# Kernel optimization log

Hardware: AMD Instinct MI355X
Metric: run time of the kernel (lower is better)

The kernel has to match this reference:

```python
import jax, jax.numpy as jnp
import numpy as np

B, T, D = 4, 4096, 1024
H, HD, K = 16, 64, 32
TAU, THRESHOLD, PULSE_BASE, N_STEPS = 0.1, 0.5, 4.0, 5


def setup_inputs() -> dict:
    key = jax.random.key(0)
    ks = jax.random.split(key, 8)
    s = 0.02
    return {
        "x": jax.random.normal(ks[0], (B, T, D), jnp.float32),
        "spectral_basis": jax.random.normal(ks[1], (B, T, K), jnp.float32) / np.sqrt(T),
        "W_qkv": jax.random.normal(ks[2], (3 * D, D), jnp.float32) * s,
        "W_out": jax.random.normal(ks[3], (D, D), jnp.float32) * s,
        "a": jnp.float32(0.7),
        "b": jnp.float32(0.8),
        "W1": jax.random.normal(ks[4], (HD // 2, HD), jnp.float32) * s,
        "b1": jnp.zeros((HD // 2,), jnp.float32),
        "W2": jax.random.normal(ks[5], (1, HD // 2), jnp.float32) * s,
        "b2": jnp.zeros((1,), jnp.float32),
        "spectral_filter": jnp.full((H, 32), 0.5, jnp.float32),
    }


def soliton_dynamics(stimulus, a, b):
    # stimulus: (B, H, K, HD); FitzHugh-Nagumo style 5-step Euler integration
    dt = 1.0 / N_STEPS
    v = jnp.zeros_like(stimulus)
    w = jnp.zeros_like(stimulus)
    stim_scale = jnp.clip(jnp.max(jnp.abs(stimulus), axis=-1, keepdims=True), 1e-06, None)
    stim_n = stimulus / stim_scale
    I = jnp.where(jnp.abs(stimulus) > THRESHOLD, stim_n, stim_n * 0.1)
    for _ in range(N_STEPS):
        dv = v - v ** 3 / 3 - w + I
        dw = (v + a - b * w) / TAU
        v = jnp.clip(v + dt * dv, -3.0, 3.0)
        w = jnp.clip(w + dt * dw, -3.0, 3.0)
    return v * stim_scale, v


def reference(x, spectral_basis, W_qkv, W_out, a, b, W1, b1, W2, b2, spectral_filter):
    Bx, Tx, Dx = x.shape
    k = spectral_basis.shape[-1]
    qkv = x @ W_qkv.T                                   # (B,T,3D)
    qkv = qkv.reshape(Bx, Tx, 3, H, HD).transpose(2, 0, 3, 1, 4)
    q, kk, v = qkv[0], qkv[1], qkv[2]                   # (B,H,T,HD)

    qm = q.mean(axis=2)                                 # (B,H,HD)
    h1 = jax.nn.silu(qm @ W1.T + b1)
    pulse_widths = PULSE_BASE + jax.nn.softplus(h1 @ W2.T + b2)[..., 0]  # (B,H)

    q_spec = jnp.einsum('bhtd,btk->bhkd', q, spectral_basis)
    k_spec = jnp.einsum('bhtd,btk->bhkd', kk, spectral_basis)
    attn_spec = jnp.einsum('bhkd,bhkd->bhk', q_spec, k_spec) / np.sqrt(HD)
    filt = jax.nn.sigmoid(spectral_filter[:, :k])       # (H,k)
    attn_spec = attn_spec * filt[None]

    stim = jnp.broadcast_to(attn_spec[..., None], (Bx, H, k, HD))
    response, state = soliton_dynamics(stim, a, b)
    response = response.mean(axis=-1)                   # (B,H,k)

    v_spec = jnp.einsum('bhtd,btk->bhkd', v, spectral_basis)
    out_spec = response[..., None] * v_spec             # (B,H,k,HD)
    out = jnp.einsum('bhkd,btk->bhtd', out_spec, spectral_basis)
    out = out.transpose(0, 2, 1, 3).reshape(Bx, Tx, Dx)
    out = out @ W_out.T
    return out, pulse_widths, response
```

## Files before the change

### kernel.cpp

```cpp
#include <hip/hip_runtime.h>

#define B_ 4
#define T_ 4096
#define D_ 1024
#define H_ 16
#define K_ 32


__device__ __forceinline__ void fma4(float4& a, float s, const float4& v){
  a.x = fmaf(s, v.x, a.x); a.y = fmaf(s, v.y, a.y);
  a.z = fmaf(s, v.z, a.z); a.w = fmaf(s, v.w, a.w);
}

__global__ __launch_bounds__(256) void reduce_g(
    const float4* __restrict__ src, float4* __restrict__ dst,
    const int n4, const int zper, const int stride4)
{
  const int g = blockIdx.y;
  int i = blockIdx.x * 256 + threadIdx.x;
  if (i >= n4) return;
  float s0 = 0.f, s1 = 0.f, s2 = 0.f, s3 = 0.f;
  const float4* p = src + (size_t)g * zper * stride4 + i;
  #pragma unroll 8
  for (int zz = 0; zz < zper; ++zz){
    float4 v = p[(size_t)zz * stride4];
    s0 += v.x; s1 += v.y; s2 += v.z; s3 += v.w;
  }
  float4 o; o.x = s0; o.y = s1; o.z = s2; o.w = s3;
  dst[(size_t)g * stride4 + i] = o;
}

__global__ __launch_bounds__(256) void reduce_zp(
    const float4* __restrict__ src, float4* __restrict__ dst,
    const int n4, const int z, const int stride4, const int total4)
{
  int i = blockIdx.x * 256 + threadIdx.x;
  if (i >= total4) return;
  if (i >= n4){
    float4 zv; zv.x = 0.f; zv.y = 0.f; zv.z = 0.f; zv.w = 0.f;
    dst[i] = zv; return;
  }
  float s0 = 0.f, s1 = 0.f, s2 = 0.f, s3 = 0.f;
  const float4* p = src + i;
  #pragma unroll 8
  for (int zz = 0; zz < z; ++zz){
    float4 v = p[(size_t)zz * stride4];
    s0 += v.x; s1 += v.y; s2 += v.z; s3 += v.w;
  }
  float4 o; o.x = s0; o.y = s1; o.z = s2; o.w = s3;
  dst[i] = o;
}

__global__ __launch_bounds__(256) void reduce_z(
    const float4* __restrict__ src, float4* __restrict__ dst,
    const int n4, const int z, const int stride4)
{
  int i = blockIdx.x * 256 + threadIdx.x;
  if (i >= n4) return;
  float s0 = 0.f, s1 = 0.f, s2 = 0.f, s3 = 0.f;
  const float4* p = src + i;
  #pragma unroll 8
  for (int zz = 0; zz < z; ++zz){
    float4 v = p[(size_t)zz * stride4];
    s0 += v.x; s1 += v.y; s2 += v.z; s3 += v.w;
  }
  float4 o; o.x = s0; o.y = s1; o.z = s2; o.w = s3;
  dst[i] = o;
}

__global__ __launch_bounds__(256) void k1_spectral_p(
    const float* __restrict__ x, const float* __restrict__ sb,
    float* __restrict__ XP)
{
  const int ct = blockIdx.x;
  const int b  = blockIdx.y;
  const int zz = blockIdx.z;
  const int t0 = zz * 64;
  const int cs = threadIdx.x & 63;
  const int kg = threadIdx.x >> 6;
  __shared__ __align__(16) float4 xt[4096];
  __shared__ __align__(16) float sbs[64][36];
  #pragma unroll
  for (int i = 0; i < 8; i++){
    int idx = threadIdx.x + i * 256;
    int t = idx >> 5, kk = idx & 31;
    sbs[t][kk] = sb[(size_t)(b * T_ + t0 + t) * K_ + kk];
  }
  const float4* xg = (const float4*)(x + (size_t)(b * T_ + t0) * D_ + ct * 256);
  float4 rv[16];
  #pragma unroll
  for (int j = 0; j < 16; j++){
    int idx = threadIdx.x + j * 256;
    int t = idx >> 6, cq = idx & 63;
    rv[j] = xg[(size_t)t * 256 + cq];
  }
  #pragma unroll
  for (int j = 0; j < 16; j++) xt[threadIdx.x + j * 256] = rv[j];
  __syncthreads();

  float4 acc[8];
  #pragma unroll
  for (int k = 0; k < 8; k++){ acc[k].x = 0.f; acc[k].y = 0.f;
                               acc[k].z = 0.f; acc[k].w = 0.f; }
  float4 am; am.x = 0.f; am.y = 0.f; am.z = 0.f; am.w = 0.f;
  #pragma unroll 4
  for (int t = 0; t < 64; ++t){
    float4 xv = xt[t * 64 + cs];
    if (kg == 0){ am.x += xv.x; am.y += xv.y; am.z += xv.z; am.w += xv.w; }
    const float4* srow = (const float4*)&sbs[t][kg * 8];
    float4 s0 = srow[0], s1 = srow[1];
    fma4(acc[0], s0.x, xv); fma4(acc[1], s0.y, xv);
    fma4(acc[2], s0.z, xv); fma4(acc[3], s0.w, xv);
    fma4(acc[4], s1.x, xv); fma4(acc[5], s1.y, xv);
    fma4(acc[6], s1.z, xv); fma4(acc[7], s1.w, xv);
  }
  const int c = ct * 256 + cs * 4;
  float* o = XP + (size_t)zz * 135168 + (size_t)(b * K_ + kg * 8) * D_ + c;
  #pragma unroll
  for (int k = 0; k < 8; k++) *(float4*)(o + (size_t)k * D_) = acc[k];
  if (kg == 0)
    *(float4*)(XP + (size_t)zz * 135168 + 131072 + b * D_ + c) = am;
}

__global__ __launch_bounds__(256) void gemm_qkv(
    const float* __restrict__ A, const float* __restrict__ W,
    float* __restrict__ Cp)
{
  __shared__ __align__(16) float As[64][68];
  __shared__ __align__(16) float Ws[64][132];
  const int nt = blockIdx.x, mt = blockIdx.y;
  const int cb = blockIdx.z * 64;
  const int sc = threadIdx.x & 63, sr = threadIdx.x >> 6;
  {
    const float* Ap = A + (size_t)(mt * 64 + sr) * 1024 + cb + sc;
    float r[16];
    #pragma unroll
    for (int i = 0; i < 16; i++) r[i] = Ap[(size_t)(i * 4) * 1024];
    #pragma unroll
    for (int i = 0; i < 16; i++) As[sc][sr + i * 4] = r[i];
  }
  {
    const float* Wp = W + (size_t)(nt * 128 + sr) * 1024 + cb + sc;
    float r[32];
    #pragma unroll
    for (int i = 0; i < 32; i++) r[i] = Wp[(size_t)(i * 4) * 1024];
    #pragma unroll
    for (int i = 0; i < 32; i++) Ws[sc][sr + i * 4] = r[i];
  }
  __syncthreads();
  const int tx = threadIdx.x & 15, ty = threadIdx.x >> 4;
  float4 acc[4][2];
  #pragma unroll
  for (int i = 0; i < 4; i++)
    #pragma unroll
    for (int j = 0; j < 2; j++){ acc[i][j].x = 0.f; acc[i][j].y = 0.f;
                                 acc[i][j].z = 0.f; acc[i][j].w = 0.f; }
  #pragma unroll 8
  for (int c = 0; c < 64; ++c){
    const float4 a4 = *(const float4*)&As[c][ty * 4];
    const float4 w0 = *(const float4*)&Ws[c][tx * 4];
    const float4 w1 = *(const float4*)&Ws[c][64 + tx * 4];
    fma4(acc[0][0], a4.x, w0); fma4(acc[0][1], a4.x, w1);
    fma4(acc[1][0], a4.y, w0); fma4(acc[1][1], a4.y, w1);
    fma4(acc[2][0], a4.z, w0); fma4(acc[2][1], a4.z, w1);
    fma4(acc[3][0], a4.w, w0); fma4(acc[3][1], a4.w, w1);
  }
  float* cp = Cp + (size_t)blockIdx.z * 589824;
  #pragma unroll
  for (int i = 0; i < 4; i++){
    float* row = cp + (size_t)(mt * 64 + ty * 4 + i) * 3072 + nt * 128;
    *(float4*)(row + tx * 4)      = acc[i][0];
    *(float4*)(row + 64 + tx * 4) = acc[i][1];
  }
}

__global__ __launch_bounds__(256) void gemm_aw_p(
    const float* __restrict__ A, const float* __restrict__ W,
    float* __restrict__ Cp, const int N, const int cPerSplit, const int MN)
{
  __shared__ __align__(16) float As[32][68];
  __shared__ __align__(16) float Ws[32][68];
  const int nt = blockIdx.x, mt = blockIdx.y;
  const int cbase = blockIdx.z * cPerSplit;
  const int tx = threadIdx.x & 15, ty = threadIdx.x >> 4;
  const int sc = threadIdx.x & 31, sr = threadIdx.x >> 5;
  float acc[4][4];
  #pragma unroll
  for (int i = 0; i < 4; i++)
    #pragma unroll
    for (int j = 0; j < 4; j++) acc[i][j] = 0.f;

  float ra[8], rw[8];
  const float* Ap = A + (size_t)(mt * 64 + sr) * 1024 + cbase + sc;
  const float* Wp = W + (size_t)(nt * 64 + sr) * 1024 + cbase + sc;
  #pragma unroll
  for (int i = 0; i < 8; i++){ ra[i] = Ap[(size_t)(i * 8) * 1024];
                               rw[i] = Wp[(size_t)(i * 8) * 1024]; }
  #pragma unroll
  for (int i = 0; i < 8; i++){ As[sc][sr + i * 8] = ra[i];
                               Ws[sc][sr + i * 8] = rw[i]; }
  __syncthreads();

  for (int cc = 32; cc < cPerSplit; cc += 32){
    #pragma unroll
    for (int i = 0; i < 8; i++){ ra[i] = Ap[(size_t)(i * 8) * 1024 + cc];
                                 rw[i] = Wp[(size_t)(i * 8) * 1024 + cc]; }
    #pragma unroll 4
    for (int c = 0; c < 32; ++c){
      const float4 a4 = *(const float4*)&As[c][ty * 4];
      const float4 w4 = *(const float4*)&Ws[c][tx * 4];
      acc[0][0] = fmaf(a4.x, w4.x, acc[0][0]);
      acc[0][1] = fmaf(a4.x, w4.y, acc[0][1]);
      acc[0][2] = fmaf(a4.x, w4.z, acc[0][2]);
      acc[0][3] = fmaf(a4.x, w4.w, acc[0][3]);
      acc[1][0] = fmaf(a4.y, w4.x, acc[1][0]);
      acc[1][1] = fmaf(a4.y, w4.y, acc[1][1]);
      acc[1][2] = fmaf(a4.y, w4.z, acc[1][2]);
      acc[1][3] = fmaf(a4.y, w4.w, acc[1][3]);
      acc[2][0] = fmaf(a4.z, w4.x, acc[2][0]);
      acc[2][1] = fmaf(a4.z, w4.y, acc[2][1]);
      acc[2][2] = fmaf(a4.z, w4.z, acc[2][2]);
      acc[2][3] = fmaf(a4.z, w4.w, acc[2][3]);
      acc[3][0] = fmaf(a4.w, w4.x, acc[3][0]);
      acc[3][1] = fmaf(a4.w, w4.y, acc[3][1]);
      acc[3][2] = fmaf(a4.w, w4.z, acc[3][2]);
      acc[3][3] = fmaf(a4.w, w4.w, acc[3][3]);
    }
    __syncthreads();
    #pragma unroll
    for (int i = 0; i < 8; i++){ As[sc][sr + i * 8] = ra[i];
                                 Ws[sc][sr + i * 8] = rw[i]; }
    __syncthreads();
  }
  #pragma unroll 4
  for (int c = 0; c < 32; ++c){
    const float4 a4 = *(const float4*)&As[c][ty * 4];
    const float4 w4 = *(const float4*)&Ws[c][tx * 4];
    acc[0][0] = fmaf(a4.x, w4.x, acc[0][0]);
    acc[0][1] = fmaf(a4.x, w4.y, acc[0][1]);
    acc[0][2] = fmaf(a4.x, w4.z, acc[0][2]);
    acc[0][3] = fmaf(a4.x, w4.w, acc[0][3]);
    acc[1][0] = fmaf(a4.y, w4.x, acc[1][0]);
    acc[1][1] = fmaf(a4.y, w4.y, acc[1][1]);
    acc[1][2] = fmaf(a4.y, w4.z, acc[1][2]);
    acc[1][3] = fmaf(a4.y, w4.w, acc[1][3]);
    acc[2][0] = fmaf(a4.z, w4.x, acc[2][0]);
    acc[2][1] = fmaf(a4.z, w4.y, acc[2][1]);
    acc[2][2] = fmaf(a4.z, w4.z, acc[2][2]);
    acc[2][3] = fmaf(a4.z, w4.w, acc[2][3]);
    acc[3][0] = fmaf(a4.w, w4.x, acc[3][0]);
    acc[3][1] = fmaf(a4.w, w4.y, acc[3][1]);
    acc[3][2] = fmaf(a4.w, w4.z, acc[3][2]);
    acc[3][3] = fmaf(a4.w, w4.w, acc[3][3]);
  }
  float* cp = Cp + (size_t)blockIdx.z * MN;
  #pragma unroll
  for (int i = 0; i < 4; i++){
    float4 o; o.x = acc[i][0]; o.y = acc[i][1]; o.z = acc[i][2]; o.w = acc[i][3];
    *(float4*)(cp + (size_t)(mt * 64 + ty * 4 + i) * N + nt * 64 + tx * 4) = o;
  }
}

__global__ __launch_bounds__(64) void k3_small(
    const float* __restrict__ qkvC,
    const float* __restrict__ W1, const float* __restrict__ b1,
    const float* __restrict__ W2, const float* __restrict__ b2,
    const float* __restrict__ filt,
    const float* __restrict__ a_in, const float* __restrict__ b_in,
    float* __restrict__ u, float* __restrict__ out_pulse,
    float* __restrict__ out_resp)
{
  const int b = blockIdx.x >> 4, h = blockIdx.x & 15;
  const int d = threadIdx.x;
  __shared__ float qm[64];
  __shared__ float h1s[32];
  __shared__ float rsp[32];
  qm[d] = qkvC[(size_t)(128 + b) * 3072 + h * 64 + d] * (1.0f / 4096.0f);
  __syncthreads();
  if (d < 32){
    float z = b1[d];
    for (int j = 0; j < 64; j++) z = fmaf(qm[j], W1[d * 64 + j], z);
    h1s[d] = z / (1.0f + __expf(-z));
  }
  __syncthreads();
  if (d == 0){
    float z2 = b2[0];
    for (int j = 0; j < 32; j++) z2 = fmaf(h1s[j], W2[j], z2);
    out_pulse[b * H_ + h] = 4.0f + log1pf(__expf(z2));
  }
  if (d < 32){
    const int k = d;
    const float* qrow = qkvC + (size_t)(b * K_ + k) * 3072 + h * 64;
    const float* krow = qrow + 1024;
    float s = 0.f;
    for (int j = 0; j < 64; j++) s = fmaf(qrow[j], krow[j], s);
    float fg = 1.0f / (1.0f + __expf(-filt[h * 32 + k]));
    s = s * 0.125f * fg;
    float av = a_in[0], bv = b_in[0];
    float sc = fmaxf(fabsf(s), 1e-6f);
    float sn = s / sc;
    float I  = (fabsf(s) > 0.5f) ? sn : 0.1f * sn;
    float v = 0.f, w = 0.f;
    #pragma unroll
    for (int it = 0; it < 5; ++it){
      float dv = v - v * v * v * (1.0f / 3.0f) - w + I;
      float dw = (v + av - bv * w) * 10.0f;
      v = fminf(fmaxf(v + 0.2f * dv, -3.0f), 3.0f);
      w = fminf(fmaxf(w + 0.2f * dw, -3.0f), 3.0f);
    }
    float r = v * sc;
    rsp[k] = r;
    out_resp[(b * H_ + h) * K_ + k] = r;
  }
  __syncthreads();
  for (int k = 0; k < 32; k++){
    u[(size_t)(b * K_ + k) * D_ + h * 64 + d] =
        rsp[k] * qkvC[(size_t)(b * K_ + k) * 3072 + 2048 + h * 64 + d];
  }
}

__global__ __launch_bounds__(256) void k4_main(
    const float* __restrict__ sb, const float* __restrict__ Mf,
    float* __restrict__ out)
{
  const int ct = blockIdx.x;
  const int yy = blockIdx.y;
  const int r0 = (yy < 28 ? yy : yy + 4) * 32;
  const int b  = r0 >> 12;
  const int w  = threadIdx.x >> 6;
  const int ls = threadIdx.x & 63;
  __shared__ __align__(16) float sbsT[32][36];
  #pragma unroll
  for (int i = 0; i < 4; i++){
    int idx = threadIdx.x + i * 256;
    int t = idx >> 5, k = idx & 31;
    sbsT[k][t] = sb[(size_t)(r0 + t) * K_ + k];
  }
  __syncthreads();
  float4 acc[8];
  #pragma unroll
  for (int i = 0; i < 8; i++){ acc[i].x = 0.f; acc[i].y = 0.f;
                               acc[i].z = 0.f; acc[i].w = 0.f; }
  const float4* Mg = (const float4*)(Mf + (size_t)b * K_ * D_);
  const int eq = ct * 64 + ls;
  #pragma unroll 8
  for (int k = 0; k < 32; ++k){
    float4 mv = Mg[(size_t)k * 256 + eq];
    const float4* srow = (const float4*)&sbsT[k][w * 8];
    float4 s0 = srow[0], s1 = srow[1];
    fma4(acc[0], s0.x, mv); fma4(acc[1], s0.y, mv);
    fma4(acc[2], s0.z, mv); fma4(acc[3], s0.w, mv);
    fma4(acc[4], s1.x, mv); fma4(acc[5], s1.y, mv);
    fma4(acc[6], s1.z, mv); fma4(acc[7], s1.w, mv);
  }
  float* op = out + (size_t)(r0 + w * 8) * D_ + eq * 4;
  #pragma unroll
  for (int i = 0; i < 8; i++)
    *(float4*)(op + (size_t)i * D_) = acc[i];
}

__global__ __launch_bounds__(256) void k4_tailp(
    const float* __restrict__ sb, const float* __restrict__ Mf,
    float* __restrict__ out)
{
  __shared__ float sbs[128][33];
  __shared__ __align__(16) float Ms[32][16];
  const int j = blockIdx.x;
  #pragma unroll
  for (int i = 0; i < 2; i++){
    int idx = threadIdx.x + i * 256;
    int k = idx >> 4, e = idx & 15;
    Ms[k][e] = Mf[(size_t)k * D_ + j * 16 + e];
  }
  #pragma unroll
  for (int i = 0; i < 16; i++){
    int idx = threadIdx.x + i * 256;
    int k = idx & 31, t = idx >> 5;
    sbs[t][k] = sb[(size_t)(896 + t) * K_ + k];
  }
  __syncthreads();
  const int t  = threadIdx.x >> 1;
  const int c0 = (threadIdx.x & 1) * 8;
  float a0 = 0.f, a1 = 0.f, a2 = 0.f, a3 = 0.f;
  float a4 = 0.f, a5 = 0.f, a6 = 0.f, a7 = 0.f;
  #pragma unroll
  for (int k = 0; k < 32; k++){
    float s = sbs[t][k];
    const float4 m0 = *(const float4*)&Ms[k][c0];
    const float4 m1 = *(const float4*)&Ms[k][c0 + 4];
    a0 = fmaf(s, m0.x, a0); a1 = fmaf(s, m0.y, a1);
    a2 = fmaf(s, m0.z, a2); a3 = fmaf(s, m0.w, a3);
    a4 = fmaf(s, m1.x, a4); a5 = fmaf(s, m1.y, a5);
    a6 = fmaf(s, m1.z, a6); a7 = fmaf(s, m1.w, a7);
  }
  float* op = out + (size_t)(896 + t) * D_ + j * 16 + c0;
  float4 o0; o0.x = a0; o0.y = a1; o0.z = a2; o0.w = a3;
  float4 o1; o1.x = a4; o1.y = a5; o1.z = a6; o1.w = a7;
  *(float4*)(op)     = o0;
  *(float4*)(op + 4) = o1;
}

extern "C" void kernel_launch(void* const* d_in, const int* in_sizes, int n_in,
                              void* d_out, int out_size, void* d_ws, size_t ws_size,
                              hipStream_t stream)
{
  const float* x    = (const float*)d_in[0];
  const float* sb   = (const float*)d_in[1];
  const float* Wqkv = (const float*)d_in[2];
  const float* Wout = (const float*)d_in[3];
  const float* a_in = (const float*)d_in[4];
  const float* b_in = (const float*)d_in[5];
  const float* W1   = (const float*)d_in[6];
  const float* b1   = (const float*)d_in[7];
  const float* W2   = (const float*)d_in[8];
  const float* b2   = (const float*)d_in[9];
  const float* filt = (const float*)d_in[10];

  float* outF = (float*)d_out;
  float* qkv  = outF + 196608;
  float* u    = outF + 786432;
  float* Mm   = outF + 917504;
  float* S    = outF + 1048576;
  float* S2   = outF + 9699328;
  float* S3   = outF + 5242880;
  float* pulse = outF + 16777216;
  float* resp  = outF + 16777280;

  k1_spectral_p<<<dim3(4, 4, 64), 256, 0, stream>>>(x, sb, S);
  reduce_g<<<dim3(132, 8), 256, 0, stream>>>((const float4*)S, (float4*)S2,
                                             33792, 8, 33792);
  reduce_zp<<<dim3(192), 256, 0, stream>>>((const float4*)S2, (float4*)outF,
                                           33792, 8, 33792, 49152);

  gemm_qkv<<<dim3(24, 3, 16), 256, 0, stream>>>(outF, Wqkv, S);
  reduce_z<<<dim3(576), 256, 0, stream>>>((const float4*)S, (float4*)qkv,
                                          147456, 16, 147456);

  k3_small<<<dim3(64), dim3(64), 0, stream>>>(qkv, W1, b1, W2, b2,
                                              filt, a_in, b_in, u,
                                              pulse, resp);

  gemm_aw_p<<<dim3(16, 2, 16), 256, 0, stream>>>(u, Wout, S, 1024, 64, 131072);
  reduce_g<<<dim3(128, 4), 256, 0, stream>>>((const float4*)S, (float4*)S3,
                                             32768, 4, 32768);
  reduce_z<<<dim3(128), 256, 0, stream>>>((const float4*)S3, (float4*)Mm,
                                          32768, 4, 32768);

  k4_main<<<dim3(4, 508), 256, 0, stream>>>(sb, Mm, outF);
  k4_tailp<<<dim3(64), 256, 0, stream>>>(sb, Mm, outF);
}
```

Baseline: 231.4 us.

## Double-step split-K chunks with register prefetch and drop intermediate reduction passes

The spectral projection kernel now covers 128 timesteps per block and the QKV GEMM covers 128 K-columns per block. Each loads its second 64-wide chunk into registers while computing on the first, then stages it through shared memory. This halves the number of split-K partial slabs, so the two-level reduce_g passes are dropped and single reduce_zp/reduce_z calls sum more partials directly. The aim is to cut partial-sum write/read traffic and kernel launches, at the cost of fewer blocks in flight and more registers per thread.

```diff
diff --git a/kernel.cpp b/kernel.cpp
--- a/kernel.cpp
+++ b/kernel.cpp
@@ -10,24 +10,6 @@
 __device__ __forceinline__ void fma4(float4& a, float s, const float4& v){
   a.x = fmaf(s, v.x, a.x); a.y = fmaf(s, v.y, a.y);
   a.z = fmaf(s, v.z, a.z); a.w = fmaf(s, v.w, a.w);
-}
-
-__global__ __launch_bounds__(256) void reduce_g(
-    const float4* __restrict__ src, float4* __restrict__ dst,
-    const int n4, const int zper, const int stride4)
-{
-  const int g = blockIdx.y;
-  int i = blockIdx.x * 256 + threadIdx.x;
-  if (i >= n4) return;
-  float s0 = 0.f, s1 = 0.f, s2 = 0.f, s3 = 0.f;
-  const float4* p = src + (size_t)g * zper * stride4 + i;
-  #pragma unroll 8
-  for (int zz = 0; zz < zper; ++zz){
-    float4 v = p[(size_t)zz * stride4];
-    s0 += v.x; s1 += v.y; s2 += v.z; s3 += v.w;
-  }
-  float4 o; o.x = s0; o.y = s1; o.z = s2; o.w = s3;
-  dst[(size_t)g * stride4 + i] = o;
 }
 
 __global__ __launch_bounds__(256) void reduce_zp(
@@ -75,28 +57,44 @@
   const int ct = blockIdx.x;
   const int b  = blockIdx.y;
   const int zz = blockIdx.z;
-  const int t0 = zz * 64;
+  const int t0 = zz * 128;
   const int cs = threadIdx.x & 63;
   const int kg = threadIdx.x >> 6;
   __shared__ __align__(16) float4 xt[4096];
   __shared__ __align__(16) float sbs[64][36];
+
+  const float4* xg = (const float4*)(x + (size_t)(b * T_ + t0) * D_ + ct * 256);
+  {
+    float4 rv[16]; float rs[8];
+    #pragma unroll
+    for (int j = 0; j < 16; j++){
+      int idx = threadIdx.x + j * 256; int t = idx >> 6, cq = idx & 63;
+      rv[j] = xg[(size_t)t * 256 + cq];
+    }
+    #pragma unroll
+    for (int i = 0; i < 8; i++){
+      int idx = threadIdx.x + i * 256; int t = idx >> 5, kk = idx & 31;
+      rs[i] = sb[(size_t)(b * T_ + t0 + t) * K_ + kk];
+    }
+    #pragma unroll
+    for (int j = 0; j < 16; j++) xt[threadIdx.x + j * 256] = rv[j];
+    #pragma unroll
+    for (int i = 0; i < 8; i++){
+      int idx = threadIdx.x + i * 256; sbs[idx >> 5][idx & 31] = rs[i];
+    }
+  }
+  __syncthreads();
+  float4 rv1[16]; float rs1[8];
+  #pragma unroll
+  for (int j = 0; j < 16; j++){
+    int idx = threadIdx.x + j * 256; int t = idx >> 6, cq = idx & 63;
+    rv1[j] = xg[(size_t)(t + 64) * 256 + cq];
+  }
   #pragma unroll
   for (int i = 0; i < 8; i++){
-    int idx = threadIdx.x + i * 256;
-    int t = idx >> 5, kk = idx & 31;
-    sbs[t][kk] = sb[(size_t)(b * T_ + t0 + t) * K_ + kk];
-  }
-  const float4* xg = (const float4*)(x + (size_t)(b * T_ + t0) * D_ + ct * 256);
-  float4 rv[16];
-  #pragma unroll
-  for (int j = 0; j < 16; j++){
-    int idx = threadIdx.x + j * 256;
-    int t = idx >> 6, cq = idx & 63;
-    rv[j] = xg[(size_t)t * 256 + cq];
-  }
-  #pragma unroll
-  for (int j = 0; j < 16; j++) xt[threadIdx.x + j * 256] = rv[j];
-  __syncthreads();
+    int idx = threadIdx.x + i * 256; int t = idx >> 5, kk = idx & 31;
+    rs1[i] = sb[(size_t)(b * T_ + t0 + 64 + t) * K_ + kk];
+  }
 
   float4 acc[8];
   #pragma unroll
@@ -114,6 +112,25 @@
     fma4(acc[4], s1.x, xv); fma4(acc[5], s1.y, xv);
     fma4(acc[6], s1.z, xv); fma4(acc[7], s1.w, xv);
   }
+  __syncthreads();
+  #pragma unroll
+  for (int j = 0; j < 16; j++) xt[threadIdx.x + j * 256] = rv1[j];
+  #pragma unroll
+  for (int i = 0; i < 8; i++){
+    int idx = threadIdx.x + i * 256; sbs[idx >> 5][idx & 31] = rs1[i];
+  }
+  __syncthreads();
+  #pragma unroll 4
+  for (int t = 0; t < 64; ++t){
+    float4 xv = xt[t * 64 + cs];
+    if (kg == 0){ am.x += xv.x; am.y += xv.y; am.z += xv.z; am.w += xv.w; }
+    const float4* srow = (const float4*)&sbs[t][kg * 8];
+    float4 s0 = srow[0], s1 = srow[1];
+    fma4(acc[0], s0.x, xv); fma4(acc[1], s0.y, xv);
+    fma4(acc[2], s0.z, xv); fma4(acc[3], s0.w, xv);
+    fma4(acc[4], s1.x, xv); fma4(acc[5], s1.y, xv);
+    fma4(acc[6], s1.z, xv); fma4(acc[7], s1.w, xv);
+  }
   const int c = ct * 256 + cs * 4;
   float* o = XP + (size_t)zz * 135168 + (size_t)(b * K_ + kg * 8) * D_ + c;
   #pragma unroll
@@ -129,25 +146,28 @@
   __shared__ __align__(16) float As[64][68];
   __shared__ __align__(16) float Ws[64][132];
   const int nt = blockIdx.x, mt = blockIdx.y;
-  const int cb = blockIdx.z * 64;
+  const int cb0 = blockIdx.z * 128;
   const int sc = threadIdx.x & 63, sr = threadIdx.x >> 6;
+  const float* Ap = A + (size_t)(mt * 64 + sr) * 1024 + cb0 + sc;
+  const float* Wp = W + (size_t)(nt * 128 + sr) * 1024 + cb0 + sc;
   {
-    const float* Ap = A + (size_t)(mt * 64 + sr) * 1024 + cb + sc;
-    float r[16];
-    #pragma unroll
-    for (int i = 0; i < 16; i++) r[i] = Ap[(size_t)(i * 4) * 1024];
-    #pragma unroll
-    for (int i = 0; i < 16; i++) As[sc][sr + i * 4] = r[i];
-  }
-  {
-    const float* Wp = W + (size_t)(nt * 128 + sr) * 1024 + cb + sc;
-    float r[32];
-    #pragma unroll
-    for (int i = 0; i < 32; i++) r[i] = Wp[(size_t)(i * 4) * 1024];
-    #pragma unroll
-    for (int i = 0; i < 32; i++) Ws[sc][sr + i * 4] = r[i];
-  }
-  __syncthreads();
+    float ra[16], rw[32];
+    #pragma unroll
+    for (int i = 0; i < 16; i++) ra[i] = Ap[(size_t)(i * 4) * 1024];
+    #pragma unroll
+    for (int i = 0; i < 32; i++) rw[i] = Wp[(size_t)(i * 4) * 1024];
+    #pragma unroll
+    for (int i = 0; i < 16; i++) As[sc][sr + i * 4] = ra[i];
+    #pragma unroll
+    for (int i = 0; i < 32; i++) Ws[sc][sr + i * 4] = rw[i];
+  }
+  __syncthreads();
+  float ra1[16], rw1[32];
+  #pragma unroll
+  for (int i = 0; i < 16; i++) ra1[i] = Ap[(size_t)(i * 4) * 1024 + 64];
+  #pragma unroll
+  for (int i = 0; i < 32; i++) rw1[i] = Wp[(size_t)(i * 4) * 1024 + 64];
+
   const int tx = threadIdx.x & 15, ty = threadIdx.x >> 4;
   float4 acc[4][2];
   #pragma unroll
@@ -155,6 +175,22 @@
     #pragma unroll
     for (int j = 0; j < 2; j++){ acc[i][j].x = 0.f; acc[i][j].y = 0.f;
                                  acc[i][j].z = 0.f; acc[i][j].w = 0.f; }
+  #pragma unroll 8
+  for (int c = 0; c < 64; ++c){
+    const float4 a4 = *(const float4*)&As[c][ty * 4];
+    const float4 w0 = *(const float4*)&Ws[c][tx * 4];
+    const float4 w1 = *(const float4*)&Ws[c][64 + tx * 4];
+    fma4(acc[0][0], a4.x, w0); fma4(acc[0][1], a4.x, w1);
+    fma4(acc[1][0], a4.y, w0); fma4(acc[1][1], a4.y, w1);
+    fma4(acc[2][0], a4.z, w0); fma4(acc[2][1], a4.z, w1);
+    fma4(acc[3][0], a4.w, w0); fma4(acc[3][1], a4.w, w1);
+  }
+  __syncthreads();
+  #pragma unroll
+  for (int i = 0; i < 16; i++) As[sc][sr + i * 4] = ra1[i];
+  #pragma unroll
+  for (int i = 0; i < 32; i++) Ws[sc][sr + i * 4] = rw1[i];
+  __syncthreads();
   #pragma unroll 8
   for (int c = 0; c < 64; ++c){
     const float4 a4 = *(const float4*)&As[c][ty * 4];
@@ -421,30 +457,24 @@
   float* u    = outF + 786432;
   float* Mm   = outF + 917504;
   float* S    = outF + 1048576;
-  float* S2   = outF + 9699328;
-  float* S3   = outF + 5242880;
   float* pulse = outF + 16777216;
   float* resp  = outF + 16777280;
 
-  k1_spectral_p<<<dim3(4, 4, 64), 256, 0, stream>>>(x, sb, S);
-  reduce_g<<<dim3(132, 8), 256, 0, stream>>>((const float4*)S, (float4*)S2,
-                                             33792, 8, 33792);
-  reduce_zp<<<dim3(192), 256, 0, stream>>>((const float4*)S2, (float4*)outF,
-                                           33792, 8, 33792, 49152);
-
-  gemm_qkv<<<dim3(24, 3, 16), 256, 0, stream>>>(outF, Wqkv, S);
+  k1_spectral_p<<<dim3(4, 4, 32), 256, 0, stream>>>(x, sb, S);
+  reduce_zp<<<dim3(192), 256, 0, stream>>>((const float4*)S, (float4*)outF,
+                                           33792, 32, 33792, 49152);
+
+  gemm_qkv<<<dim3(24, 3, 8), 256, 0, stream>>>(outF, Wqkv, S);
   reduce_z<<<dim3(576), 256, 0, stream>>>((const float4*)S, (float4*)qkv,
-                                          147456, 16, 147456);
+                                          147456, 8, 147456);
 
   k3_small<<<dim3(64), dim3(64), 0, stream>>>(qkv, W1, b1, W2, b2,
                                               filt, a_in, b_in, u,
                                               pulse, resp);
 
   gemm_aw_p<<<dim3(16, 2, 16), 256, 0, stream>>>(u, Wout, S, 1024, 64, 131072);
-  reduce_g<<<dim3(128, 4), 256, 0, stream>>>((const float4*)S, (float4*)S3,
-                                             32768, 4, 32768);
-  reduce_z<<<dim3(128), 256, 0, stream>>>((const float4*)S3, (float4*)Mm,
-                                          32768, 4, 32768);
+  reduce_z<<<dim3(128), 256, 0, stream>>>((const float4*)S, (float4*)Mm,
+                                          32768, 16, 32768);
 
   k4_main<<<dim3(4, 508), 256, 0, stream>>>(sb, Mm, outF);
   k4_tailp<<<dim3(64), 256, 0, stream>>>(sb, Mm, outF);
```

Measured after the change: 251.3 us. +8.6%, slower.
